# Kernel optimization log

Measured on AMD Instinct MI355X. Metric: run time of the kernel, lower is better.

Reference implementation:

```python
import jax, jax.numpy as jnp
import numpy as np


def _gelu(x):
    return jax.nn.gelu(x, approximate=False)


def _conv2d(x, w, b, pad=0, dil=1, groups=1):
    y = jax.lax.conv_general_dilated(
        x, w, (1, 1), [(pad, pad), (pad, pad)], rhs_dilation=(dil, dil),
        dimension_numbers=('NCHW', 'OIHW', 'NCHW'), feature_group_count=groups)
    return y + b[None, :, None, None]


def _ln_last(x, g, b, eps=1e-5):
    m = jnp.mean(x, -1, keepdims=True)
    v = jnp.var(x, -1, keepdims=True)
    return (x - m) * jax.lax.rsqrt(v + eps) * g + b


def _ln2d(x, g, b, eps=1e-5):
    # LayerNorm over channel dim of NCHW
    m = jnp.mean(x, 1, keepdims=True)
    v = jnp.var(x, 1, keepdims=True)
    return (x - m) * jax.lax.rsqrt(v + eps) * g[None, :, None, None] + b[None, :, None, None]


def _bilinear(x, py, px):
    # x: [B,C,H,W]; py,px: [B,H,W] float sample coords; zero outside
    B, C, H, W = x.shape
    y0 = jnp.floor(py)
    x0 = jnp.floor(px)
    wy = py - y0
    wx = px - x0
    xf = x.reshape(B, C, H * W)

    def g(yi, xi):
        valid = ((yi >= 0) & (yi < H) & (xi >= 0) & (xi < W)).astype(x.dtype)
        yc = jnp.clip(yi, 0, H - 1).astype(jnp.int32)
        xc = jnp.clip(xi, 0, W - 1).astype(jnp.int32)
        idx = (yc * W + xc).reshape(B, 1, H * W)
        v = jnp.take_along_axis(xf, idx, axis=2).reshape(B, C, H, W)
        return v * valid[:, None]

    return (g(y0, x0) * ((1 - wy) * (1 - wx))[:, None]
            + g(y0, x0 + 1) * ((1 - wy) * wx)[:, None]
            + g(y0 + 1, x0) * (wy * (1 - wx))[:, None]
            + g(y0 + 1, x0 + 1) * (wy * wx)[:, None])


def _deform_dw(x, ow, ob, w, b, dil):
    # modulated deformable depthwise 3x3 conv, offset_groups=1
    B, C, H, W = x.shape
    pad = dil
    off = _conv2d(x, ow, ob, pad=pad, dil=dil)          # [B,27,H,W]
    ox, oy, m = jnp.split(off, 3, axis=1)               # each [B,9,H,W]
    m = jax.nn.sigmoid(m)
    ys = jnp.arange(H, dtype=x.dtype)[None, :, None]
    xs = jnp.arange(W, dtype=x.dtype)[None, None, :]
    acc = jnp.zeros_like(x)
    for ki in range(3):
        for kj in range(3):
            kk = ki * 3 + kj
            py = ys - pad + ki * dil + oy[:, kk]
            px = xs - pad + kj * dil + ox[:, kk]
            s = _bilinear(x, py, px)                    # [B,C,H,W]
            acc = acc + s * m[:, kk][:, None] * w[:, 0, ki, kj][None, :, None, None]
    return acc + b[None, :, None, None]


def _forward(image_embed, inter_prototypes, intra_prototypes, masks,
             proj_w, proj_b, lin_w, lin_b, tok_g, tok_b, alpha,
             in_w, in_b, off0_w, off0_b, dw0_w, dw0_b,
             off1_w, off1_b, dw1_w, dw1_b, cv_w, cv_b, ln_g, ln_b,
             op0_w, op0_b, op1_w, op1_b, op2_w, op2_b,
             out0_w, out0_b, out1_w, out1_b):
    C = image_embed.shape[1]
    scale = C ** -0.5
    # prototype tokens [B,Q,C]
    pt = jnp.einsum('bqc,bnc->bqn', inter_prototypes, intra_prototypes)
    t = jnp.concatenate([inter_prototypes, pt], axis=-1) @ proj_w + proj_b
    t = _gelu(t) @ lin_w + lin_b
    t = _ln_last(t, tok_g, tok_b)
    # mask gating of image features
    pe = jnp.einsum('bnc,bnhw->bchw', intra_prototypes, masks)
    img = image_embed * pe + image_embed
    # DeformAttn
    x = _gelu(_conv2d(img, in_w, in_b))
    a = _deform_dw(x, off0_w, off0_b, dw0_w, dw0_b, dil=1)
    a = _deform_dw(a, off1_w, off1_b, dw1_w, dw1_b, dil=3)
    a = _conv2d(a, cv_w, cv_b)
    x = x * a + img
    x = _ln2d(x, ln_g, ln_b)
    y = _conv2d(x, op0_w, op0_b)
    y = _gelu(_conv2d(y, op1_w, op1_b, pad=1, groups=C))
    y = _conv2d(y, op2_w, op2_b)
    dense = y + x
    # prototype cross-attention over 8 tokens
    attn = jnp.einsum('bchw,bqc->bqhw', dense, t) * scale
    attn = jax.nn.softmax(attn, axis=1)
    attn = jnp.einsum('bqhw,bqc->bchw', attn, t)
    attn = attn + dense * alpha[None, :, None, None]
    o = _gelu(_conv2d(attn, out0_w, out0_b))
    o = _conv2d(o, out1_w, out1_b)
    return o


def setup_inputs():
    key = jax.random.key(0)
    ks = jax.random.split(key, 40)
    B, C, H, W, Q, N = 16, 256, 64, 64, 8, 9
    f32 = jnp.float32

    def rn(k, shp, s=1.0):
        return jax.random.normal(k, shp, f32) * s

    inp = {
        'image_embed': rn(ks[0], (B, C, H, W)),
        'inter_prototypes': rn(ks[1], (B, Q, C)),
        'intra_prototypes': rn(ks[2], (B, N, C)),
        'masks': jax.random.uniform(ks[3], (B, N, H, W), f32),
        'proj_w': rn(ks[4], (C + N, C), 0.02), 'proj_b': jnp.zeros((C,), f32),
        'lin_w': rn(ks[5], (C, C), 0.02), 'lin_b': jnp.zeros((C,), f32),
        'tok_g': 1.0 + rn(ks[6], (C,), 0.05), 'tok_b': rn(ks[7], (C,), 0.05),
        'alpha': jnp.ones((C,), f32) * 0.001,
        'in_w': rn(ks[8], (C, C, 1, 1), 0.02), 'in_b': jnp.zeros((C,), f32),
        'off0_w': rn(ks[9], (27, C, 3, 3), 0.01), 'off0_b': rn(ks[10], (27,), 0.01),
        'dw0_w': rn(ks[11], (C, 1, 3, 3), 0.2), 'dw0_b': jnp.zeros((C,), f32),
        'off1_w': rn(ks[12], (27, C, 3, 3), 0.01), 'off1_b': rn(ks[13], (27,), 0.01),
        'dw1_w': rn(ks[14], (C, 1, 3, 3), 0.2), 'dw1_b': jnp.zeros((C,), f32),
        'cv_w': rn(ks[15], (C, C, 1, 1), 0.02), 'cv_b': jnp.zeros((C,), f32),
        'ln_g': 1.0 + rn(ks[16], (C,), 0.05), 'ln_b': rn(ks[17], (C,), 0.05),
        'op0_w': rn(ks[18], (C, C, 1, 1), 0.02), 'op0_b': jnp.zeros((C,), f32),
        'op1_w': rn(ks[19], (C, 1, 3, 3), 0.2), 'op1_b': jnp.zeros((C,), f32),
        'op2_w': rn(ks[20], (C, C, 1, 1), 0.02), 'op2_b': jnp.zeros((C,), f32),
        'out0_w': rn(ks[21], (C // 2, C, 1, 1), 0.02), 'out0_b': jnp.zeros((C // 2,), f32),
        'out1_w': rn(ks[22], (C, C // 2, 1, 1), 0.02), 'out1_b': jnp.zeros((C,), f32),
    }
    return inp


def reference(image_embed, inter_prototypes, intra_prototypes, masks,
              proj_w, proj_b, lin_w, lin_b, tok_g, tok_b, alpha,
              in_w, in_b, off0_w, off0_b, dw0_w, dw0_b,
              off1_w, off1_b, dw1_w, dw1_b, cv_w, cv_b, ln_g, ln_b,
              op0_w, op0_b, op1_w, op1_b, op2_w, op2_b,
              out0_w, out0_b, out1_w, out1_b):
    return _forward(image_embed, inter_prototypes, intra_prototypes, masks,
                    proj_w, proj_b, lin_w, lin_b, tok_g, tok_b, alpha,
                    in_w, in_b, off0_w, off0_b, dw0_w, dw0_b,
                    off1_w, off1_b, dw1_w, dw1_b, cv_w, cv_b, ln_g, ln_b,
                    op0_w, op0_b, op1_w, op1_b, op2_w, op2_b,
                    out0_w, out0_b, out1_w, out1_b)
```

## Files before the change

kernel.cpp:

```cpp
#include <hip/hip_runtime.h>
#include <math.h>

#define BB 16
#define CC 256
#define HH 64
#define WW 64
#define HWs 4096
#define PP 65536
#define QQ 8
#define NN 9

typedef _Float16 half8_t __attribute__((ext_vector_type(8)));
typedef _Float16 half4_t __attribute__((ext_vector_type(4)));
typedef float floatx4 __attribute__((ext_vector_type(4)));

__device__ __forceinline__ float gelu_f(float x) {
    return 0.5f * x * (1.0f + erff(x * 0.70710678118654752f));
}

__global__ void prep_weights_kernel(const float* __restrict__ off0_w, const float* __restrict__ off1_w,
                                    const float* __restrict__ dw0_w, const float* __restrict__ dw1_w,
                                    const float* __restrict__ op1_w,
                                    const float* __restrict__ in_w, const float* __restrict__ cv_w,
                                    const float* __restrict__ op0_w, const float* __restrict__ op2_w,
                                    const float* __restrict__ out0_w, const float* __restrict__ out1_w,
                                    float* __restrict__ dwt0, float* __restrict__ dwt1,
                                    float* __restrict__ op1t,
                                    _Float16* __restrict__ wh_in, _Float16* __restrict__ wh_cv,
                                    _Float16* __restrict__ wh_op0, _Float16* __restrict__ wh_op2,
                                    _Float16* __restrict__ wh_out0, _Float16* __restrict__ wh_out1,
                                    _Float16* __restrict__ whoff0, _Float16* __restrict__ whoff1) {
    int i = blockIdx.x * 256 + threadIdx.x;
    if (i < 9*256) {
        int c = i & 255;
        int tap = i >> 8;
        dwt0[i] = dw0_w[c*9 + tap];
        dwt1[i] = dw1_w[c*9 + tap];
        op1t[i] = op1_w[c*9 + tap];
    }
    if (i < 65536) {
        wh_in[i]  = (_Float16)in_w[i];
        wh_cv[i]  = (_Float16)cv_w[i];
        wh_op0[i] = (_Float16)op0_w[i];
        wh_op2[i] = (_Float16)op2_w[i];
    }
    if (i < 32768) {
        wh_out0[i] = (_Float16)out0_w[i];
        wh_out1[i] = (_Float16)out1_w[i];
    }
    if (i < 9*32*256) {
        int ci = i & 255;
        int k32 = (i >> 8) & 31;
        int tap = i >> 13;
        float v0 = 0.f, v1 = 0.f;
        if (k32 < 27) {
            v0 = off0_w[(k32*256 + ci)*9 + tap];
            v1 = off1_w[(k32*256 + ci)*9 + tap];
        }
        whoff0[i] = (_Float16)v0;
        whoff1[i] = (_Float16)v1;
    }
}

__global__ void token_kernel(const float* __restrict__ inter, const float* __restrict__ intra,
                             const float* __restrict__ proj_w, const float* __restrict__ proj_b,
                             const float* __restrict__ lin_w, const float* __restrict__ lin_b,
                             const float* __restrict__ tok_g, const float* __restrict__ tok_b,
                             float* __restrict__ t_out) {
    int bq = blockIdx.x;
    int b = bq >> 3, q = bq & 7;
    int c = threadIdx.x;
    __shared__ float inter_s[256];
    __shared__ float pt_s[9];
    __shared__ float g_s[256];
    __shared__ float red[256];
    __shared__ float stat[2];
    inter_s[c] = inter[(b*QQ + q)*CC + c];
    __syncthreads();
    for (int n = 0; n < 9; n++) {
        red[c] = inter_s[c] * intra[(b*NN + n)*CC + c];
        __syncthreads();
        for (int s = 128; s > 0; s >>= 1) {
            if (c < s) red[c] += red[c + s];
            __syncthreads();
        }
        if (c == 0) pt_s[n] = red[0];
        __syncthreads();
    }
    float u = proj_b[c];
    for (int k = 0; k < 256; k++) u += inter_s[k] * proj_w[k*CC + c];
    for (int n = 0; n < 9; n++) u += pt_s[n] * proj_w[(256 + n)*CC + c];
    g_s[c] = gelu_f(u);
    __syncthreads();
    float v = lin_b[c];
    for (int k = 0; k < 256; k++) v += g_s[k] * lin_w[k*CC + c];
    red[c] = v;
    __syncthreads();
    for (int s = 128; s > 0; s >>= 1) { if (c < s) red[c] += red[c + s]; __syncthreads(); }
    if (c == 0) stat[0] = red[0] * (1.0f/256.0f);
    __syncthreads();
    float m = stat[0];
    red[c] = (v - m)*(v - m);
    __syncthreads();
    for (int s = 128; s > 0; s >>= 1) { if (c < s) red[c] += red[c + s]; __syncthreads(); }
    if (c == 0) stat[1] = red[0] * (1.0f/256.0f);
    __syncthreads();
    float var = stat[1];
    float r = rsqrtf(var + 1e-5f);
    t_out[(b*QQ + q)*CC + c] = (v - m) * r * tok_g[c] + tok_b[c];
}

__global__ void img_pe_kernel(const float* __restrict__ ie, const float* __restrict__ intra,
                              const float* __restrict__ masks, float* __restrict__ img) {
    int b = blockIdx.z;
    int c0 = blockIdx.y * 32;
    int s0 = blockIdx.x * 32;
    __shared__ float tile[32][33];
    __shared__ float intra_s[9][32];
    __shared__ float mask_s[9][32];
    int tx = threadIdx.x, ty = threadIdx.y;
    int t = ty*32 + tx;
    for (int i = t; i < 288; i += 256) {
        int n = i >> 5, j = i & 31;
        intra_s[n][j] = intra[(b*NN + n)*CC + c0 + j];
        mask_s[n][j]  = masks[(b*NN + n)*HWs + s0 + j];
    }
    __syncthreads();
    #pragma unroll
    for (int r = 0; r < 4; r++) {
        int cl = ty + 8*r;
        float val = ie[(b*CC + c0 + cl)*HWs + s0 + tx];
        float pe = 0.f;
        #pragma unroll
        for (int n = 0; n < 9; n++) pe += intra_s[n][cl] * mask_s[n][tx];
        tile[cl][tx] = val * (1.0f + pe);
    }
    __syncthreads();
    #pragma unroll
    for (int r = 0; r < 4; r++) {
        int sl = ty + 8*r;
        img[(b*HWs + s0 + sl)*CC + c0 + tx] = tile[tx][sl];
    }
}

template<int CI, int CO, int ACT, bool RES, bool INH, bool XH>
__global__ void __launch_bounds__(256) conv1x1_mfma(const void* __restrict__ in, const _Float16* __restrict__ Wh,
        const float* __restrict__ bias, const float* __restrict__ res, float* __restrict__ out,
        _Float16* __restrict__ outh) {
    constexpr int KS = CI/32;
    constexpr int NF = CO/64;
    constexpr int LDR = CI + 8;
    __shared__ __align__(16) _Float16 a_lds[64*LDR];
    int t = threadIdx.x;
    int wid = t >> 6, lane = t & 63;
    int quad = lane >> 4, l16 = lane & 15;
    int p0 = blockIdx.x * 64;
    if (INH) {
        const half8_t* inh = (const half8_t*)in + (size_t)p0*(CI/8);
        for (int i = t; i < 64*(CI/8); i += 256) {
            int r = i/(CI/8), c8 = i%(CI/8);
            *(half8_t*)&a_lds[r*LDR + c8*8] = inh[i];
        }
    } else {
        const float4* inf = (const float4*)in + (size_t)p0*(CI/4);
        for (int i = t; i < 64*(CI/4); i += 256) {
            float4 v = inf[i];
            half4_t hv; hv[0]=(_Float16)v.x; hv[1]=(_Float16)v.y; hv[2]=(_Float16)v.z; hv[3]=(_Float16)v.w;
            int r = i/(CI/4), c4 = i%(CI/4);
            *(half4_t*)&a_lds[r*LDR + c4*4] = hv;
        }
    }
    __syncthreads();
    int n0 = wid*(CO/4);
    floatx4 acc[4][NF];
    #pragma unroll
    for (int mf = 0; mf < 4; mf++)
        #pragma unroll
        for (int nf = 0; nf < NF; nf++)
            #pragma unroll
            for (int r = 0; r < 4; r++) acc[mf][nf][r] = 0.f;
    for (int ks = 0; ks < KS; ks++) {
        int k = ks*32 + quad*8;
        half8_t a[4];
        #pragma unroll
        for (int mf = 0; mf < 4; mf++)
            a[mf] = *(const half8_t*)&a_lds[(mf*16 + l16)*LDR + k];
        half8_t bfr[NF];
        #pragma unroll
        for (int nf = 0; nf < NF; nf++)
            bfr[nf] = *(const half8_t*)&Wh[(size_t)(n0 + nf*16 + l16)*CI + k];
        #pragma unroll
        for (int mf = 0; mf < 4; mf++)
            #pragma unroll
            for (int nf = 0; nf < NF; nf++)
                acc[mf][nf] = __builtin_amdgcn_mfma_f32_16x16x32_f16(a[mf], bfr[nf], acc[mf][nf], 0, 0, 0);
    }
    #pragma unroll
    for (int nf = 0; nf < NF; nf++) {
        int co = n0 + nf*16 + l16;
        float bs = bias[co];
        #pragma unroll
        for (int mf = 0; mf < 4; mf++) {
            #pragma unroll
            for (int r = 0; r < 4; r++) {
                int p = p0 + mf*16 + quad*4 + r;
                float v = acc[mf][nf][r] + bs;
                if (ACT) v = gelu_f(v);
                if (RES) v += res[(size_t)p*CO + co];
                out[(size_t)p*CO + co] = v;
                if (XH) outh[(size_t)p*CO + co] = (_Float16)v;
            }
        }
    }
}

template<int DIL>
__global__ void __launch_bounds__(256) off_conv_mfma(const _Float16* __restrict__ x, const _Float16* __restrict__ Wh,
        const float* __restrict__ bias, float* __restrict__ off) {
    constexpr int LDR = 264;
    __shared__ __align__(16) _Float16 xs[70*LDR];
    int raw = blockIdx.x;
    int bh = (raw & 7) * 128 + (raw >> 3);
    int b = bh >> 6, h = bh & 63;
    int t = threadIdx.x;
    int wid = t >> 6, lane = t & 63;
    int quad = lane >> 4, l16 = lane & 15;
    for (int i = t; i < 6*LDR; i += 256) {
        int r = i/LDR, c = i%LDR;
        int row = (r < 3) ? r : (64 + r);
        xs[row*LDR + c] = (_Float16)0.f;
    }
    floatx4 acc[2];
    #pragma unroll
    for (int nf = 0; nf < 2; nf++)
        #pragma unroll
        for (int r = 0; r < 4; r++) acc[nf][r] = 0.f;
    for (int ki = 0; ki < 3; ki++) {
        int hrow = h + (ki - 1)*DIL;
        __syncthreads();
        if (hrow >= 0 && hrow < 64) {
            const half8_t* row = (const half8_t*)(x + ((size_t)(b*64 + hrow)*64) * 256);
            for (int i = t; i < 2048; i += 256) {
                int r = i >> 5, c8 = i & 31;
                *(half8_t*)&xs[(r + 3)*LDR + c8*8] = row[r*32 + c8];
            }
        } else {
            half8_t z = (half8_t)((_Float16)0.f);
            for (int i = t; i < 2048; i += 256) {
                int r = i >> 5, c8 = i & 31;
                *(half8_t*)&xs[(r + 3)*LDR + c8*8] = z;
            }
        }
        __syncthreads();
        #pragma unroll
        for (int kj = 0; kj < 3; kj++) {
            const _Float16* wt = Wh + (size_t)(ki*3 + kj)*32*256;
            int wrow = wid*16 + l16 + (kj - 1)*DIL + 3;
            #pragma unroll
            for (int cs = 0; cs < 8; cs++) {
                int k = cs*32 + quad*8;
                half8_t a = *(const half8_t*)&xs[wrow*LDR + k];
                half8_t b0 = *(const half8_t*)&wt[(size_t)l16*256 + k];
                half8_t b1 = *(const half8_t*)&wt[(size_t)(16 + l16)*256 + k];
                acc[0] = __builtin_amdgcn_mfma_f32_16x16x32_f16(a, b0, acc[0], 0, 0, 0);
                acc[1] = __builtin_amdgcn_mfma_f32_16x16x32_f16(a, b1, acc[1], 0, 0, 0);
            }
        }
    }
    int pbase = (b*64 + h)*64;
    #pragma unroll
    for (int nf = 0; nf < 2; nf++) {
        int kcol = nf*16 + l16;
        if (kcol < 27) {
            float bs = bias[kcol];
            #pragma unroll
            for (int r = 0; r < 4; r++) {
                int w = wid*16 + quad*4 + r;
                off[(size_t)(pbase + w)*27 + kcol] = acc[nf][r] + bs;
            }
        }
    }
}

template<int DIL>
__global__ void __launch_bounds__(256) deform_kernel(const _Float16* __restrict__ src, const float* __restrict__ off,
        const float* __restrict__ dwt, const float* __restrict__ dwb, _Float16* __restrict__ out) {
    int raw = blockIdx.x;
    int swz = (raw & 7) * 256 + (raw >> 3);
    int whalf = swz & 1;
    int bh = swz >> 1;
    int b = bh >> 6, h = bh & 63;
    int t = threadIdx.x;
    int c4 = t & 63;
    int ps = t >> 6;

    __shared__ float wq[288*4];
    __shared__ int   iq[288*4];

    for (int j = t; j < 288; j += 256) {
        int lw = j / 9;
        int kk = j - lw*9;
        int w = whalf*32 + lw;
        int p = (b*64 + h)*64 + w;
        const float* op = off + (size_t)p*27;
        float ox = op[kk];
        float oy = op[9 + kk];
        float mm = op[18 + kk];
        mm = 1.0f / (1.0f + expf(-mm));
        int ki = kk / 3, kj = kk - ki*3;
        float py = (float)(h - DIL + ki*DIL) + oy;
        float px = (float)(w - DIL + kj*DIL) + ox;
        float y0f = floorf(py), x0f = floorf(px);
        float wy = py - y0f, wx = px - x0f;
        int y0 = (int)y0f, x0 = (int)x0f;
        int y1 = y0 + 1, x1 = x0 + 1;
        float w00 = (1.f - wy)*(1.f - wx)*mm;
        float w01 = (1.f - wy)*wx*mm;
        float w10 = wy*(1.f - wx)*mm;
        float w11 = wy*wx*mm;
        bool yv0 = (y0 >= 0) && (y0 < 64);
        bool yv1 = (y1 >= 0) && (y1 < 64);
        bool xv0 = (x0 >= 0) && (x0 < 64);
        bool xv1 = (x1 >= 0) && (x1 < 64);
        int y0c = min(max(y0, 0), 63), y1c = min(max(y1, 0), 63);
        int x0c = min(max(x0, 0), 63), x1c = min(max(x1, 0), 63);
        int base = b*4096;
        wq[j*4+0] = (yv0 && xv0) ? w00 : 0.f;
        wq[j*4+1] = (yv0 && xv1) ? w01 : 0.f;
        wq[j*4+2] = (yv1 && xv0) ? w10 : 0.f;
        wq[j*4+3] = (yv1 && xv1) ? w11 : 0.f;
        iq[j*4+0] = base + y0c*64 + x0c;
        iq[j*4+1] = base + y0c*64 + x1c;
        iq[j*4+2] = base + y1c*64 + x0c;
        iq[j*4+3] = base + y1c*64 + x1c;
    }
    __syncthreads();

    float4 dwv[9];
    #pragma unroll
    for (int kk = 0; kk < 9; kk++) dwv[kk] = ((const float4*)dwt)[kk*64 + c4];
    float4 bv = ((const float4*)dwb)[c4];
    const half4_t* srcf = (const half4_t*)src;
    for (int i = 0; i < 8; i++) {
        int lw = ps*8 + i;
        int w = whalf*32 + lw;
        int p = (b*64 + h)*64 + w;
        float4 acc = make_float4(0.f,0.f,0.f,0.f);
        #pragma unroll
        for (int kk = 0; kk < 9; kk++) {
            int q = (lw*9 + kk)*4;
            float a0 = wq[q+0], a1 = wq[q+1], a2 = wq[q+2], a3 = wq[q+3];
            int i0 = iq[q+0], i1 = iq[q+1], i2 = iq[q+2], i3 = iq[q+3];
            half4_t v0 = srcf[(size_t)i0*64 + c4];
            half4_t v1 = srcf[(size_t)i1*64 + c4];
            half4_t v2 = srcf[(size_t)i2*64 + c4];
            half4_t v3 = srcf[(size_t)i3*64 + c4];
            float sx = (float)v0[0]*a0 + (float)v1[0]*a1 + (float)v2[0]*a2 + (float)v3[0]*a3;
            float sy = (float)v0[1]*a0 + (float)v1[1]*a1 + (float)v2[1]*a2 + (float)v3[1]*a3;
            float sz = (float)v0[2]*a0 + (float)v1[2]*a1 + (float)v2[2]*a2 + (float)v3[2]*a3;
            float sw = (float)v0[3]*a0 + (float)v1[3]*a1 + (float)v2[3]*a2 + (float)v3[3]*a3;
            acc.x += sx * dwv[kk].x;
            acc.y += sy * dwv[kk].y;
            acc.z += sz * dwv[kk].z;
            acc.w += sw * dwv[kk].w;
        }
        half4_t o4;
        o4[0] = (_Float16)(acc.x + bv.x);
        o4[1] = (_Float16)(acc.y + bv.y);
        o4[2] = (_Float16)(acc.z + bv.z);
        o4[3] = (_Float16)(acc.w + bv.w);
        ((half4_t*)out)[(size_t)p*64 + c4] = o4;
    }
}

__global__ void __launch_bounds__(256) gate_ln_kernel(const float* __restrict__ x, const float* __restrict__ a,
        const float* __restrict__ img, const float* __restrict__ g, const float* __restrict__ bb,
        float* __restrict__ out) {
    int t = threadIdx.x;
    int lane = t & 63;
    int wv = t >> 6;
    int p = blockIdx.x*4 + wv;
    float4 xv = ((const float4*)x)[p*64 + lane];
    float4 av = ((const float4*)a)[p*64 + lane];
    float4 iv = ((const float4*)img)[p*64 + lane];
    float4 v;
    v.x = xv.x*av.x + iv.x; v.y = xv.y*av.y + iv.y;
    v.z = xv.z*av.z + iv.z; v.w = xv.w*av.w + iv.w;
    float s = v.x + v.y + v.z + v.w;
    float s2 = v.x*v.x + v.y*v.y + v.z*v.z + v.w*v.w;
    #pragma unroll
    for (int o = 1; o < 64; o <<= 1) { s += __shfl_xor(s, o); s2 += __shfl_xor(s2, o); }
    float m = s * (1.f/256.f);
    float var = s2 * (1.f/256.f) - m*m;
    float r = rsqrtf(var + 1e-5f);
    float4 gv = ((const float4*)g)[lane];
    float4 bv = ((const float4*)bb)[lane];
    float4 o4;
    o4.x = (v.x - m)*r*gv.x + bv.x;
    o4.y = (v.y - m)*r*gv.y + bv.y;
    o4.z = (v.z - m)*r*gv.z + bv.z;
    o4.w = (v.w - m)*r*gv.w + bv.w;
    ((float4*)out)[p*64 + lane] = o4;
}

__global__ void __launch_bounds__(256) dw3x3_kernel(const float* __restrict__ in, const float* __restrict__ wt,
        const float* __restrict__ bias, float* __restrict__ out) {
    int raw = blockIdx.x;
    int swz = (raw & 7) * 2048 + (raw >> 3);
    int gid = swz*256 + threadIdx.x;
    int c4 = gid & 63;
    int p = gid >> 6;
    int w = p & 63;
    int h = (p >> 6) & 63;
    int b = p >> 12;
    float4 acc = ((const float4*)bias)[c4];
    #pragma unroll
    for (int ki = 0; ki < 3; ki++) {
        int hh = h + ki - 1;
        if (hh < 0 || hh >= 64) continue;
        #pragma unroll
        for (int kj = 0; kj < 3; kj++) {
            int wwp = w + kj - 1;
            if (wwp < 0 || wwp >= 64) continue;
            float4 v = ((const float4*)in)[((b*64 + hh)*64 + wwp)*64 + c4];
            float4 wv = ((const float4*)wt)[(ki*3 + kj)*64 + c4];
            acc.x += v.x*wv.x; acc.y += v.y*wv.y; acc.z += v.z*wv.z; acc.w += v.w*wv.w;
        }
    }
    acc.x = gelu_f(acc.x); acc.y = gelu_f(acc.y); acc.z = gelu_f(acc.z); acc.w = gelu_f(acc.w);
    ((float4*)out)[p*64 + c4] = acc;
}

__global__ void __launch_bounds__(256) attn_kernel(const float* __restrict__ dense, const float* __restrict__ tok,
        const float* __restrict__ alpha, float* __restrict__ out) {
    __shared__ float4 t_s[8*64];
    __shared__ float4 al_s[64];
    int bh = blockIdx.x;
    int b = bh >> 6, h = bh & 63;
    int t = threadIdx.x;
    for (int i = t; i < 512; i += 256) t_s[i] = ((const float4*)tok)[b*512 + i];
    if (t < 64) al_s[t] = ((const float4*)alpha)[t];
    __syncthreads();
    int lane = t & 63, ps = t >> 6;
    for (int i = 0; i < 16; i++) {
        int w = ps*16 + i;
        int p = (b*64 + h)*64 + w;
        float4 dv = ((const float4*)dense)[p*64 + lane];
        float sc[8];
        #pragma unroll
        for (int q = 0; q < 8; q++) {
            float4 tv = t_s[q*64 + lane];
            float partial = dv.x*tv.x + dv.y*tv.y + dv.z*tv.z + dv.w*tv.w;
            #pragma unroll
            for (int o = 1; o < 64; o <<= 1) partial += __shfl_xor(partial, o);
            sc[q] = partial * 0.0625f;
        }
        float mx = sc[0];
        #pragma unroll
        for (int q = 1; q < 8; q++) mx = fmaxf(mx, sc[q]);
        float e[8]; float denom = 0.f;
        #pragma unroll
        for (int q = 0; q < 8; q++) { e[q] = expf(sc[q] - mx); denom += e[q]; }
        float inv = 1.0f / denom;
        float4 al = al_s[lane];
        float4 o4;
        o4.x = dv.x*al.x; o4.y = dv.y*al.y; o4.z = dv.z*al.z; o4.w = dv.w*al.w;
        #pragma unroll
        for (int q = 0; q < 8; q++) {
            float wq = e[q]*inv;
            float4 tv = t_s[q*64 + lane];
            o4.x += wq*tv.x; o4.y += wq*tv.y; o4.z += wq*tv.z; o4.w += wq*tv.w;
        }
        ((float4*)out)[p*64 + lane] = o4;
    }
}

__global__ void nhwc_to_nchw_kernel(const float* __restrict__ in, float* __restrict__ out) {
    int b = blockIdx.z;
    int c0 = blockIdx.y*32, s0 = blockIdx.x*32;
    __shared__ float tile[32][33];
    int tx = threadIdx.x, ty = threadIdx.y;
    #pragma unroll
    for (int r = 0; r < 4; r++) {
        int sl = ty + 8*r;
        tile[tx][sl] = in[(b*HWs + s0 + sl)*CC + c0 + tx];
    }
    __syncthreads();
    #pragma unroll
    for (int r = 0; r < 4; r++) {
        int cl = ty + 8*r;
        out[(b*CC + c0 + cl)*HWs + s0 + tx] = tile[cl][tx];
    }
}

extern "C" void kernel_launch(void* const* d_in, const int* in_sizes, int n_in,
                              void* d_out, int out_size, void* d_ws, size_t ws_size,
                              hipStream_t stream) {
    const float* image_embed = (const float*)d_in[0];
    const float* inter_p     = (const float*)d_in[1];
    const float* intra_p     = (const float*)d_in[2];
    const float* masks       = (const float*)d_in[3];
    const float* proj_w      = (const float*)d_in[4];
    const float* proj_b      = (const float*)d_in[5];
    const float* lin_w       = (const float*)d_in[6];
    const float* lin_b       = (const float*)d_in[7];
    const float* tok_g       = (const float*)d_in[8];
    const float* tok_b       = (const float*)d_in[9];
    const float* alpha       = (const float*)d_in[10];
    const float* in_w        = (const float*)d_in[11];
    const float* in_b        = (const float*)d_in[12];
    const float* off0_w      = (const float*)d_in[13];
    const float* off0_b      = (const float*)d_in[14];
    const float* dw0_w       = (const float*)d_in[15];
    const float* dw0_b       = (const float*)d_in[16];
    const float* off1_w      = (const float*)d_in[17];
    const float* off1_b      = (const float*)d_in[18];
    const float* dw1_w       = (const float*)d_in[19];
    const float* dw1_b       = (const float*)d_in[20];
    const float* cv_w        = (const float*)d_in[21];
    const float* cv_b        = (const float*)d_in[22];
    const float* ln_g        = (const float*)d_in[23];
    const float* ln_b        = (const float*)d_in[24];
    const float* op0_w       = (const float*)d_in[25];
    const float* op0_b       = (const float*)d_in[26];
    const float* op1_w       = (const float*)d_in[27];
    const float* op1_b       = (const float*)d_in[28];
    const float* op2_w       = (const float*)d_in[29];
    const float* op2_b       = (const float*)d_in[30];
    const float* out0_w      = (const float*)d_in[31];
    const float* out0_b      = (const float*)d_in[32];
    const float* out1_w      = (const float*)d_in[33];
    const float* out1_b      = (const float*)d_in[34];
    (void)ws_size; (void)in_sizes; (void)n_in; (void)out_size;

    float* ws = (float*)d_ws;
    const size_t BIG = (size_t)PP * CC;
    float* A   = ws;
    float* Bb  = A + BIG;
    float* Cb  = Bb + BIG;
    float* D   = (float*)d_out;
    float* OFF = Cb + BIG;
    float* TOK = OFF + (size_t)PP*27;
    float* DWT0 = TOK + BB*QQ*CC;
    float* DWT1 = DWT0 + 9*256;
    float* OP1T = DWT1 + 9*256;
    _Float16* WH_IN   = (_Float16*)(OP1T + 9*256);
    _Float16* WH_CV   = WH_IN + 65536;
    _Float16* WH_OP0  = WH_CV + 65536;
    _Float16* WH_OP2  = WH_OP0 + 65536;
    _Float16* WH_OUT0 = WH_OP2 + 65536;
    _Float16* WH_OUT1 = WH_OUT0 + 32768;
    _Float16* WHOFF0  = WH_OUT1 + 32768;
    _Float16* WHOFF1  = WHOFF0 + 9*32*256;
    _Float16* XH  = (_Float16*)d_out;
    _Float16* A1H = (_Float16*)Cb;
    _Float16* A2H = XH;

    prep_weights_kernel<<<(9*32*256 + 255)/256, 256, 0, stream>>>(
        off0_w, off1_w, dw0_w, dw1_w, op1_w,
        in_w, cv_w, op0_w, op2_w, out0_w, out1_w,
        DWT0, DWT1, OP1T,
        WH_IN, WH_CV, WH_OP0, WH_OP2, WH_OUT0, WH_OUT1, WHOFF0, WHOFF1);
    token_kernel<<<BB*QQ, 256, 0, stream>>>(inter_p, intra_p, proj_w, proj_b,
                                            lin_w, lin_b, tok_g, tok_b, TOK);
    img_pe_kernel<<<dim3(HWs/32, CC/32, BB), dim3(32,8), 0, stream>>>(image_embed, intra_p, masks, A);
    conv1x1_mfma<256,256,1,false,false,true><<<PP/64, 256, 0, stream>>>(A, WH_IN, in_b, nullptr, Bb, XH);
    off_conv_mfma<1><<<BB*HH, 256, 0, stream>>>(XH, WHOFF0, off0_b, OFF);
    deform_kernel<1><<<BB*HH*2, 256, 0, stream>>>(XH, OFF, DWT0, dw0_b, A1H);
    off_conv_mfma<3><<<BB*HH, 256, 0, stream>>>(A1H, WHOFF1, off1_b, OFF);
    deform_kernel<3><<<BB*HH*2, 256, 0, stream>>>(A1H, OFF, DWT1, dw1_b, A2H);
    conv1x1_mfma<256,256,0,false,true,false><<<PP/64, 256, 0, stream>>>(A2H, WH_CV, cv_b, nullptr, Cb, nullptr);
    gate_ln_kernel<<<PP/4, 256, 0, stream>>>(Bb, Cb, A, ln_g, ln_b, A);
    conv1x1_mfma<256,256,0,false,false,false><<<PP/64, 256, 0, stream>>>(A, WH_OP0, op0_b, nullptr, Bb, nullptr);
    dw3x3_kernel<<<PP*64/256, 256, 0, stream>>>(Bb, OP1T, op1_b, Cb);
    conv1x1_mfma<256,256,0,true,false,false><<<PP/64, 256, 0, stream>>>(Cb, WH_OP2, op2_b, A, D, nullptr);
    attn_kernel<<<BB*HH, 256, 0, stream>>>(D, TOK, alpha, Bb);
    conv1x1_mfma<256,128,1,false,false,false><<<PP/64, 256, 0, stream>>>(Bb, WH_OUT0, out0_b, nullptr, Cb, nullptr);
    conv1x1_mfma<128,256,0,false,false,false><<<PP/64, 256, 0, stream>>>(Cb, WH_OUT1, out1_b, nullptr, A, nullptr);
    nhwc_to_nchw_kernel<<<dim3(HWs/32, CC/32, BB), dim3(32,8), 0, stream>>>(A, (float*)d_out);
}
```

Baseline: 929.2 us.

## Store intermediate activations in fp16 across the pipeline and scalarize deform gather offsets

Converts most intermediate activation buffers (gate/LN, op0, dw3x3, op2 with residual, attention, out0) from fp32 to fp16. The 1x1 MFMA convs now read fp16 inputs directly and emit fp16 outputs, with buffer aliasing reorganized to match, which cuts memory traffic between the many bandwidth-bound stages. The deform kernel stores its bilinear weights and indices as float4/int4 in shared memory and pre-shifts the indices into byte offsets. It also reads them via readfirstlane so the gather uses scalar base addresses. The trade-off is fp16 rounding of intermediates, including the LN output used as the residual, which may reduce accuracy.

```diff
diff --git a/kernel.cpp b/kernel.cpp
--- a/kernel.cpp
+++ b/kernel.cpp
@@ -143,9 +143,9 @@
     }
 }
 
-template<int CI, int CO, int ACT, bool RES, bool INH, bool XH>
+template<int CI, int CO, int ACT, int RES, bool INH, int OUT>
 __global__ void __launch_bounds__(256) conv1x1_mfma(const void* __restrict__ in, const _Float16* __restrict__ Wh,
-        const float* __restrict__ bias, const float* __restrict__ res, float* __restrict__ out,
+        const float* __restrict__ bias, const void* __restrict__ res, float* __restrict__ out,
         _Float16* __restrict__ outh) {
     constexpr int KS = CI/32;
     constexpr int NF = CO/64;
@@ -206,9 +206,10 @@
                 int p = p0 + mf*16 + quad*4 + r;
                 float v = acc[mf][nf][r] + bs;
                 if (ACT) v = gelu_f(v);
-                if (RES) v += res[(size_t)p*CO + co];
-                out[(size_t)p*CO + co] = v;
-                if (XH) outh[(size_t)p*CO + co] = (_Float16)v;
+                if (RES == 1) v += ((const float*)res)[(size_t)p*CO + co];
+                if (RES == 2) v += (float)((const _Float16*)res)[(size_t)p*CO + co];
+                if (OUT == 0 || OUT == 2) out[(size_t)p*CO + co] = v;
+                if (OUT == 1 || OUT == 2) outh[(size_t)p*CO + co] = (_Float16)v;
             }
         }
     }
@@ -294,8 +295,8 @@
     int c4 = t & 63;
     int ps = t >> 6;
 
-    __shared__ float wq[288*4];
-    __shared__ int   iq[288*4];
+    __shared__ float4 wq4[288];
+    __shared__ int4   iq4[288];
 
     for (int j = t; j < 288; j += 256) {
         int lw = j / 9;
@@ -325,14 +326,18 @@
         int y0c = min(max(y0, 0), 63), y1c = min(max(y1, 0), 63);
         int x0c = min(max(x0, 0), 63), x1c = min(max(x1, 0), 63);
         int base = b*4096;
-        wq[j*4+0] = (yv0 && xv0) ? w00 : 0.f;
-        wq[j*4+1] = (yv0 && xv1) ? w01 : 0.f;
-        wq[j*4+2] = (yv1 && xv0) ? w10 : 0.f;
-        wq[j*4+3] = (yv1 && xv1) ? w11 : 0.f;
-        iq[j*4+0] = base + y0c*64 + x0c;
-        iq[j*4+1] = base + y0c*64 + x1c;
-        iq[j*4+2] = base + y1c*64 + x0c;
-        iq[j*4+3] = base + y1c*64 + x1c;
+        float4 wv;
+        wv.x = (yv0 && xv0) ? w00 : 0.f;
+        wv.y = (yv0 && xv1) ? w01 : 0.f;
+        wv.z = (yv1 && xv0) ? w10 : 0.f;
+        wv.w = (yv1 && xv1) ? w11 : 0.f;
+        wq4[j] = wv;
+        int4 iv;
+        iv.x = (base + y0c*64 + x0c) << 9;
+        iv.y = (base + y0c*64 + x1c) << 9;
+        iv.z = (base + y1c*64 + x0c) << 9;
+        iv.w = (base + y1c*64 + x1c) << 9;
+        iq4[j] = iv;
     }
     __syncthreads();
 
@@ -340,7 +345,7 @@
     #pragma unroll
     for (int kk = 0; kk < 9; kk++) dwv[kk] = ((const float4*)dwt)[kk*64 + c4];
     float4 bv = ((const float4*)dwb)[c4];
-    const half4_t* srcf = (const half4_t*)src;
+    const char* srcb = (const char*)src + (size_t)c4*8;
     for (int i = 0; i < 8; i++) {
         int lw = ps*8 + i;
         int w = whalf*32 + lw;
@@ -348,17 +353,21 @@
         float4 acc = make_float4(0.f,0.f,0.f,0.f);
         #pragma unroll
         for (int kk = 0; kk < 9; kk++) {
-            int q = (lw*9 + kk)*4;
-            float a0 = wq[q+0], a1 = wq[q+1], a2 = wq[q+2], a3 = wq[q+3];
-            int i0 = iq[q+0], i1 = iq[q+1], i2 = iq[q+2], i3 = iq[q+3];
-            half4_t v0 = srcf[(size_t)i0*64 + c4];
-            half4_t v1 = srcf[(size_t)i1*64 + c4];
-            half4_t v2 = srcf[(size_t)i2*64 + c4];
-            half4_t v3 = srcf[(size_t)i3*64 + c4];
-            float sx = (float)v0[0]*a0 + (float)v1[0]*a1 + (float)v2[0]*a2 + (float)v3[0]*a3;
-            float sy = (float)v0[1]*a0 + (float)v1[1]*a1 + (float)v2[1]*a2 + (float)v3[1]*a3;
-            float sz = (float)v0[2]*a0 + (float)v1[2]*a1 + (float)v2[2]*a2 + (float)v3[2]*a3;
-            float sw = (float)v0[3]*a0 + (float)v1[3]*a1 + (float)v2[3]*a2 + (float)v3[3]*a3;
+            int j = lw*9 + kk;
+            float4 wv = wq4[j];
+            int4 iv = iq4[j];
+            int o0 = __builtin_amdgcn_readfirstlane(iv.x);
+            int o1 = __builtin_amdgcn_readfirstlane(iv.y);
+            int o2 = __builtin_amdgcn_readfirstlane(iv.z);
+            int o3 = __builtin_amdgcn_readfirstlane(iv.w);
+            half4_t v0 = *(const half4_t*)(srcb + o0);
+            half4_t v1 = *(const half4_t*)(srcb + o1);
+            half4_t v2 = *(const half4_t*)(srcb + o2);
+            half4_t v3 = *(const half4_t*)(srcb + o3);
+            float sx = (float)v0[0]*wv.x + (float)v1[0]*wv.y + (float)v2[0]*wv.z + (float)v3[0]*wv.w;
+            float sy = (float)v0[1]*wv.x + (float)v1[1]*wv.y + (float)v2[1]*wv.z + (float)v3[1]*wv.w;
+            float sz = (float)v0[2]*wv.x + (float)v1[2]*wv.y + (float)v2[2]*wv.z + (float)v3[2]*wv.w;
+            float sw = (float)v0[3]*wv.x + (float)v1[3]*wv.y + (float)v2[3]*wv.z + (float)v3[3]*wv.w;
             acc.x += sx * dwv[kk].x;
             acc.y += sy * dwv[kk].y;
             acc.z += sz * dwv[kk].z;
@@ -373,19 +382,21 @@
     }
 }
 
-__global__ void __launch_bounds__(256) gate_ln_kernel(const float* __restrict__ x, const float* __restrict__ a,
+__global__ void __launch_bounds__(256) gate_ln_kernel(const _Float16* __restrict__ x, const _Float16* __restrict__ a,
         const float* __restrict__ img, const float* __restrict__ g, const float* __restrict__ bb,
-        float* __restrict__ out) {
+        _Float16* __restrict__ out) {
     int t = threadIdx.x;
     int lane = t & 63;
     int wv = t >> 6;
     int p = blockIdx.x*4 + wv;
-    float4 xv = ((const float4*)x)[p*64 + lane];
-    float4 av = ((const float4*)a)[p*64 + lane];
+    half4_t xh = ((const half4_t*)x)[p*64 + lane];
+    half4_t ah = ((const half4_t*)a)[p*64 + lane];
     float4 iv = ((const float4*)img)[p*64 + lane];
     float4 v;
-    v.x = xv.x*av.x + iv.x; v.y = xv.y*av.y + iv.y;
-    v.z = xv.z*av.z + iv.z; v.w = xv.w*av.w + iv.w;
+    v.x = (float)xh[0]*(float)ah[0] + iv.x;
+    v.y = (float)xh[1]*(float)ah[1] + iv.y;
+    v.z = (float)xh[2]*(float)ah[2] + iv.z;
+    v.w = (float)xh[3]*(float)ah[3] + iv.w;
     float s = v.x + v.y + v.z + v.w;
     float s2 = v.x*v.x + v.y*v.y + v.z*v.z + v.w*v.w;
     #pragma unroll
@@ -395,16 +406,16 @@
     float r = rsqrtf(var + 1e-5f);
     float4 gv = ((const float4*)g)[lane];
     float4 bv = ((const float4*)bb)[lane];
-    float4 o4;
-    o4.x = (v.x - m)*r*gv.x + bv.x;
-    o4.y = (v.y - m)*r*gv.y + bv.y;
-    o4.z = (v.z - m)*r*gv.z + bv.z;
-    o4.w = (v.w - m)*r*gv.w + bv.w;
-    ((float4*)out)[p*64 + lane] = o4;
-}
-
-__global__ void __launch_bounds__(256) dw3x3_kernel(const float* __restrict__ in, const float* __restrict__ wt,
-        const float* __restrict__ bias, float* __restrict__ out) {
+    half4_t o4;
+    o4[0] = (_Float16)((v.x - m)*r*gv.x + bv.x);
+    o4[1] = (_Float16)((v.y - m)*r*gv.y + bv.y);
+    o4[2] = (_Float16)((v.z - m)*r*gv.z + bv.z);
+    o4[3] = (_Float16)((v.w - m)*r*gv.w + bv.w);
+    ((half4_t*)out)[p*64 + lane] = o4;
+}
+
+__global__ void __launch_bounds__(256) dw3x3_kernel(const _Float16* __restrict__ in, const float* __restrict__ wt,
+        const float* __restrict__ bias, _Float16* __restrict__ out) {
     int raw = blockIdx.x;
     int swz = (raw & 7) * 2048 + (raw >> 3);
     int gid = swz*256 + threadIdx.x;
@@ -422,17 +433,22 @@
         for (int kj = 0; kj < 3; kj++) {
             int wwp = w + kj - 1;
             if (wwp < 0 || wwp >= 64) continue;
-            float4 v = ((const float4*)in)[((b*64 + hh)*64 + wwp)*64 + c4];
+            half4_t v = ((const half4_t*)in)[((b*64 + hh)*64 + wwp)*64 + c4];
             float4 wv = ((const float4*)wt)[(ki*3 + kj)*64 + c4];
-            acc.x += v.x*wv.x; acc.y += v.y*wv.y; acc.z += v.z*wv.z; acc.w += v.w*wv.w;
-        }
-    }
-    acc.x = gelu_f(acc.x); acc.y = gelu_f(acc.y); acc.z = gelu_f(acc.z); acc.w = gelu_f(acc.w);
-    ((float4*)out)[p*64 + c4] = acc;
-}
-
-__global__ void __launch_bounds__(256) attn_kernel(const float* __restrict__ dense, const float* __restrict__ tok,
-        const float* __restrict__ alpha, float* __restrict__ out) {
+            acc.x += (float)v[0]*wv.x; acc.y += (float)v[1]*wv.y;
+            acc.z += (float)v[2]*wv.z; acc.w += (float)v[3]*wv.w;
+        }
+    }
+    half4_t o4;
+    o4[0] = (_Float16)gelu_f(acc.x);
+    o4[1] = (_Float16)gelu_f(acc.y);
+    o4[2] = (_Float16)gelu_f(acc.z);
+    o4[3] = (_Float16)gelu_f(acc.w);
+    ((half4_t*)out)[p*64 + c4] = o4;
+}
+
+__global__ void __launch_bounds__(256) attn_kernel(const _Float16* __restrict__ dense, const float* __restrict__ tok,
+        const float* __restrict__ alpha, _Float16* __restrict__ out) {
     __shared__ float4 t_s[8*64];
     __shared__ float4 al_s[64];
     int bh = blockIdx.x;
@@ -445,7 +461,9 @@
     for (int i = 0; i < 16; i++) {
         int w = ps*16 + i;
         int p = (b*64 + h)*64 + w;
-        float4 dv = ((const float4*)dense)[p*64 + lane];
+        half4_t dh = ((const half4_t*)dense)[(size_t)p*64 + lane];
+        float4 dv;
+        dv.x = (float)dh[0]; dv.y = (float)dh[1]; dv.z = (float)dh[2]; dv.w = (float)dh[3];
         float sc[8];
         #pragma unroll
         for (int q = 0; q < 8; q++) {
@@ -471,7 +489,10 @@
             float4 tv = t_s[q*64 + lane];
             o4.x += wq*tv.x; o4.y += wq*tv.y; o4.z += wq*tv.z; o4.w += wq*tv.w;
         }
-        ((float4*)out)[p*64 + lane] = o4;
+        half4_t oh;
+        oh[0] = (_Float16)o4.x; oh[1] = (_Float16)o4.y;
+        oh[2] = (_Float16)o4.z; oh[3] = (_Float16)o4.w;
+        ((half4_t*)out)[(size_t)p*64 + lane] = oh;
     }
 }
 
@@ -538,7 +559,6 @@
     float* A   = ws;
     float* Bb  = A + BIG;
     float* Cb  = Bb + BIG;
-    float* D   = (float*)d_out;
     float* OFF = Cb + BIG;
     float* TOK = OFF + (size_t)PP*27;
     float* DWT0 = TOK + BB*QQ*CC;
@@ -552,9 +572,16 @@
     _Float16* WH_OUT1 = WH_OUT0 + 32768;
     _Float16* WHOFF0  = WH_OUT1 + 32768;
     _Float16* WHOFF1  = WHOFF0 + 9*32*256;
-    _Float16* XH  = (_Float16*)d_out;
-    _Float16* A1H = (_Float16*)Cb;
-    _Float16* A2H = XH;
+    _Float16* XH   = (_Float16*)Bb;
+    _Float16* A1H  = XH + (size_t)PP*CC;
+    _Float16* A2H  = (_Float16*)Cb;
+    _Float16* AH   = A2H + (size_t)PP*CC;
+    _Float16* XLNH = (_Float16*)d_out;
+    _Float16* Y0H  = (_Float16*)A;
+    _Float16* Y1H  = Y0H + (size_t)PP*CC;
+    _Float16* DENH = (_Float16*)Cb;
+    _Float16* ATH  = (_Float16*)Bb;
+    _Float16* O0H  = (_Float16*)Cb + (size_t)PP*CC;
 
     prep_weights_kernel<<<(9*32*256 + 255)/256, 256, 0, stream>>>(
         off0_w, off1_w, dw0_w, dw1_w, op1_w,
@@ -564,18 +591,18 @@
     token_kernel<<<BB*QQ, 256, 0, stream>>>(inter_p, intra_p, proj_w, proj_b,
                                             lin_w, lin_b, tok_g, tok_b, TOK);
     img_pe_kernel<<<dim3(HWs/32, CC/32, BB), dim3(32,8), 0, stream>>>(image_embed, intra_p, masks, A);
-    conv1x1_mfma<256,256,1,false,false,true><<<PP/64, 256, 0, stream>>>(A, WH_IN, in_b, nullptr, Bb, XH);
+    conv1x1_mfma<256,256,1,0,false,1><<<PP/64, 256, 0, stream>>>(A, WH_IN, in_b, nullptr, nullptr, XH);
     off_conv_mfma<1><<<BB*HH, 256, 0, stream>>>(XH, WHOFF0, off0_b, OFF);
     deform_kernel<1><<<BB*HH*2, 256, 0, stream>>>(XH, OFF, DWT0, dw0_b, A1H);
     off_conv_mfma<3><<<BB*HH, 256, 0, stream>>>(A1H, WHOFF1, off1_b, OFF);
     deform_kernel<3><<<BB*HH*2, 256, 0, stream>>>(A1H, OFF, DWT1, dw1_b, A2H);
-    conv1x1_mfma<256,256,0,false,true,false><<<PP/64, 256, 0, stream>>>(A2H, WH_CV, cv_b, nullptr, Cb, nullptr);
-    gate_ln_kernel<<<PP/4, 256, 0, stream>>>(Bb, Cb, A, ln_g, ln_b, A);
-    conv1x1_mfma<256,256,0,false,false,false><<<PP/64, 256, 0, stream>>>(A, WH_OP0, op0_b, nullptr, Bb, nullptr);
-    dw3x3_kernel<<<PP*64/256, 256, 0, stream>>>(Bb, OP1T, op1_b, Cb);
-    conv1x1_mfma<256,256,0,true,false,false><<<PP/64, 256, 0, stream>>>(Cb, WH_OP2, op2_b, A, D, nullptr);
-    attn_kernel<<<BB*HH, 256, 0, stream>>>(D, TOK, alpha, Bb);
-    conv1x1_mfma<256,128,1,false,false,false><<<PP/64, 256, 0, stream>>>(Bb, WH_OUT0, out0_b, nullptr, Cb, nullptr);
-    conv1x1_mfma<128,256,0,false,false,false><<<PP/64, 256, 0, stream>>>(Cb, WH_OUT1, out1_b, nullptr, A, nullptr);
+    conv1x1_mfma<256,256,0,0,true,1><<<PP/64, 256, 0, stream>>>(A2H, WH_CV, cv_b, nullptr, nullptr, AH);
+    gate_ln_kernel<<<PP/4, 256, 0, stream>>>(XH, AH, A, ln_g, ln_b, XLNH);
+    conv1x1_mfma<256,256,0,0,true,1><<<PP/64, 256, 0, stream>>>(XLNH, WH_OP0, op0_b, nullptr, nullptr, Y0H);
+    dw3x3_kernel<<<PP*64/256, 256, 0, stream>>>(Y0H, OP1T, op1_b, Y1H);
+    conv1x1_mfma<256,256,0,2,true,1><<<PP/64, 256, 0, stream>>>(Y1H, WH_OP2, op2_b, XLNH, nullptr, DENH);
+    attn_kernel<<<BB*HH, 256, 0, stream>>>(DENH, TOK, alpha, ATH);
+    conv1x1_mfma<256,128,1,0,true,1><<<PP/64, 256, 0, stream>>>(ATH, WH_OUT0, out0_b, nullptr, nullptr, O0H);
+    conv1x1_mfma<128,256,0,0,true,0><<<PP/64, 256, 0, stream>>>(O0H, WH_OUT1, out1_b, nullptr, A, nullptr);
     nhwc_to_nchw_kernel<<<dim3(HWs/32, CC/32, BB), dim3(32,8), 0, stream>>>(A, (float*)d_out);
 }
```

Measured after the change: 914.0 us. About the same (-1.6%).
